# Kernel optimization log

Measured on AMD Instinct MI355X. Metric: run time of the kernel, lower is better.

## Reference

```python
import jax, jax.numpy as jnp
import numpy as np
import math

N = 50000      # nodes
E = 800000     # edges
IN = 64        # in_channels
HID = 128      # hidden_channels
OUT = 64       # out_channels
RATIO = 0.8
K = int(math.ceil(RATIO * N))  # 40000 nodes kept after TopKPooling


def setup_inputs() -> dict:
    key = jax.random.key(0)
    ks = jax.random.split(key, 12)
    x = jax.random.normal(ks[0], (N, IN), jnp.float32)
    edge_index = jax.random.randint(ks[1], (2, E), 0, N, dtype=jnp.int32)
    batch = jnp.zeros((N,), jnp.int32)  # single graph

    def glorot(k, fi, fo):
        return jax.random.normal(k, (fi, fo), jnp.float32) * (1.0 / np.sqrt(fi))

    W1 = glorot(ks[2], IN, HID);  b1 = jnp.zeros((HID,), jnp.float32)
    pool_w = jax.random.normal(ks[3], (HID,), jnp.float32) * (1.0 / np.sqrt(HID))
    W2 = glorot(ks[4], HID, OUT); b2 = jnp.zeros((OUT,), jnp.float32)
    W3 = glorot(ks[5], OUT, HID); b3 = jnp.zeros((HID,), jnp.float32)
    W4 = glorot(ks[6], HID, IN);  b4 = jnp.zeros((IN,), jnp.float32)
    return dict(x=x, edge_index=edge_index, batch=batch,
                W1=W1, b1=b1, pool_w=pool_w, W2=W2, b2=b2,
                W3=W3, b3=b3, W4=W4, b4=b4)


def gcn_conv(x, src, dst, ew, W, b, n):
    """PyG GCNConv: D^{-1/2}(A+I)D^{-1/2} X W + b; ew is a 0/1 edge mask."""
    h = x @ W                                             # [n, d_out]
    deg = 1.0 + jax.ops.segment_sum(ew, dst, num_segments=n)  # self-loop adds 1
    dis = jax.lax.rsqrt(deg)
    norm = dis[src] * dis[dst] * ew                       # [E]
    agg = jax.ops.segment_sum(norm[:, None] * h[src], dst, num_segments=n)
    agg = agg + h * (dis * dis)[:, None]                  # self-loop: norm = 1/deg
    return agg + b


def reference(x, edge_index, batch, W1, b1, pool_w, W2, b2, W3, b3, W4, b4):
    src, dst = edge_index[0], edge_index[1]
    ew = jnp.ones((E,), x.dtype)

    # conv1 + relu
    h = jax.nn.relu(gcn_conv(x, src, dst, ew, W1, b1, N))

    # TopKPooling(ratio=0.8): score = tanh(x.w/||w||), keep top-K, scale x by score
    score = jnp.tanh(h @ pool_w / jnp.linalg.norm(pool_w))  # [N]
    vals, perm = jax.lax.top_k(score, K)
    hp = h[perm] * vals[:, None]                            # [K, HID]
    # remap edges to pooled node ids; drop edges touching removed nodes via mask
    new_idx = jnp.full((N,), -1, jnp.int32).at[perm].set(jnp.arange(K, dtype=jnp.int32))
    ns, nd = new_idx[src], new_idx[dst]
    valid = ((ns >= 0) & (nd >= 0)).astype(x.dtype)
    ns = jnp.maximum(ns, 0)
    nd = jnp.maximum(nd, 0)

    h2 = jax.nn.relu(gcn_conv(hp, ns, nd, valid, W2, b2, K))
    h3 = jax.nn.relu(gcn_conv(h2, ns, nd, valid, W3, b3, K))
    h4 = gcn_conv(h3, ns, nd, valid, W4, b4, K)             # [K, IN]

    # global_mean_pool over the (single) graph -> [1, IN]
    return jnp.mean(h4, axis=0, keepdims=True)
```

## Files before the change

### kernel.cpp

```cpp
#include <hip/hip_runtime.h>
#include <hip/hip_bf16.h>
#include <stdint.h>

#define N_NODES 50000
#define N_EDGES 800000
#define K_KEEP  40000
#define BKT     196
#define BCAP    6144

typedef unsigned long long u64;
typedef unsigned int u32;
typedef unsigned short u16;
typedef __hip_bfloat16 bf16;
typedef __hip_bfloat162 bf16x2;
typedef __attribute__((ext_vector_type(8))) short short8;
typedef __attribute__((ext_vector_type(8))) unsigned short ushort8;
typedef __attribute__((ext_vector_type(4))) float f32x4;

struct Ctl {
  u64 prefix;
  u32 kremain;
  u32 cnt;
  float inv_norm;
  u32 isfp32;
  u32 done;
  u32 pad;
  u32 gen;
  u32 done2;
  u32 hist[256];
};

__device__ __forceinline__ float bf2f(bf16 v) { return __bfloat162float(v); }
__device__ __forceinline__ float bfbits2f(unsigned short u) {
  return __uint_as_float(((u32)u) << 16);
}
__device__ __forceinline__ float loadF(const void* p, size_t i, bool f32) {
  return f32 ? ((const float*)p)[i] : bf2f(((const bf16*)p)[i]);
}
__device__ __forceinline__ short f2bf_bits(float f) {
  bf16 t = __float2bfloat16(f);
  return *(const short*)&t;
}

__device__ __forceinline__ void gather_row8(const ushort8* __restrict__ H, int d, int lane,
                                            const int* __restrict__ rowstart,
                                            const int* __restrict__ len,
                                            const int* __restrict__ csr,
                                            const float* __restrict__ dis,
                                            int relusrc, float* acc)
{
  float dd = dis[d];
  float sw = dd * dd;
  ushort8 v = H[(size_t)d * 8 + lane];
  #pragma unroll
  for (int c = 0; c < 8; ++c) {
    float t = bfbits2f(v[c]);
    if (relusrc) t = fmaxf(t, 0.f);
    acc[c] = t * sw;
  }
  int i = rowstart[d];
  int i1 = len ? (i + len[d]) : rowstart[d + 1];
  for (; i + 4 <= i1; i += 4) {
    int s0 = csr[i], s1 = csr[i + 1], s2 = csr[i + 2], s3 = csr[i + 3];
    float w0 = dd * dis[s0], w1 = dd * dis[s1], w2 = dd * dis[s2], w3 = dd * dis[s3];
    ushort8 v0 = H[(size_t)s0 * 8 + lane];
    ushort8 v1 = H[(size_t)s1 * 8 + lane];
    ushort8 v2 = H[(size_t)s2 * 8 + lane];
    ushort8 v3 = H[(size_t)s3 * 8 + lane];
    #pragma unroll
    for (int c = 0; c < 8; ++c) {
      float x0 = bfbits2f(v0[c]), x1 = bfbits2f(v1[c]);
      float x2 = bfbits2f(v2[c]), x3 = bfbits2f(v3[c]);
      if (relusrc) {
        x0 = fmaxf(x0, 0.f); x1 = fmaxf(x1, 0.f);
        x2 = fmaxf(x2, 0.f); x3 = fmaxf(x3, 0.f);
      }
      acc[c] += w0 * x0 + w1 * x1 + w2 * x2 + w3 * x3;
    }
  }
  for (; i < i1; ++i) {
    int s = csr[i];
    float w = dd * dis[s];
    ushort8 vv = H[(size_t)s * 8 + lane];
    #pragma unroll
    for (int c = 0; c < 8; ++c) {
      float xx = bfbits2f(vv[c]);
      if (relusrc) xx = fmaxf(xx, 0.f);
      acc[c] += w * xx;
    }
  }
}


__global__ void init_kernel(const unsigned short* __restrict__ x16,
                            int* __restrict__ bucket_cur, int* __restrict__ detcnt, Ctl* ctl) {
  __shared__ u32 dsh[256];
  int i = blockIdx.x * 256 + threadIdx.x;
  if (i < BKT) bucket_cur[i] = i * BCAP;
  if (blockIdx.x == 0) {
    ctl->hist[threadIdx.x] = 0u;
    if (threadIdx.x == 0) {
      ctl->prefix = 0ull; ctl->kremain = K_KEEP; ctl->cnt = 0u;
      ctl->done = 0u; ctl->pad = 0u; ctl->gen = 0u; ctl->done2 = 0u;
    }
  }
  if (blockIdx.x < 64) {
    int base = blockIdx.x * 2048;
    u32 c = 0;
    for (int j = threadIdx.x; j < 2048; j += 256) {
      u32 h = x16[base + j];
      if ((h & 0x7F80u) == 0x7F80u) c++;
    }
    dsh[threadIdx.x] = c;
    __syncthreads();
    for (int s = 128; s > 0; s >>= 1) {
      if (threadIdx.x < s) dsh[threadIdx.x] += dsh[threadIdx.x + s];
      __syncthreads();
    }
    if (threadIdx.x == 0) detcnt[blockIdx.x] = (int)dsh[0];
  }
}


__global__ void bucket_scatter_kernel(const int* __restrict__ src, const int* __restrict__ dst,
                                      int* __restrict__ bucket_cur, u32* __restrict__ bucketbuf,
                                      const void* __restrict__ x, u32* __restrict__ xbf,
                                      const int* __restrict__ detcnt, const void* __restrict__ pw,
                                      Ctl* ctl)
{
  __shared__ u32 hist[BKT];
  __shared__ u32 base[BKT];
  __shared__ int f32sh;
  __shared__ float ns[128];
  const int tid = threadIdx.x;
  const int e0 = blockIdx.x * 2048;

  if (tid < 64) {
    int dc = detcnt[tid];
    for (int off = 32; off; off >>= 1) dc += __shfl_down(dc, off);
    if (tid == 0) f32sh = (dc >= 16) ? 1 : 0;
  }
  for (int t = tid; t < BKT; t += 256) hist[t] = 0;
  __syncthreads();
  const bool f32in = f32sh != 0;

  #pragma unroll
  for (int j = 0; j < 8; ++j) {
    int e = e0 + j * 256 + tid;
    if (e < N_EDGES) atomicAdd(&hist[dst[e] >> 8], 1u);
  }
  __syncthreads();
  for (int t = tid; t < BKT; t += 256) {
    u32 c = hist[t];
    base[t] = c ? (u32)atomicAdd(&bucket_cur[t], (int)c) : 0u;
    hist[t] = 0;
  }
  __syncthreads();
  #pragma unroll
  for (int j = 0; j < 8; ++j) {
    int e = e0 + j * 256 + tid;
    if (e < N_EDGES) {
      int d = dst[e];
      int b = d >> 8;
      u32 pos = base[b] + atomicAdd(&hist[b], 1u);
      bucketbuf[pos] = ((u32)src[e] << 8) | (u32)(d & 255);
    }
  }
  if (f32in) {
    const int p0 = blockIdx.x * 4096;
    const float2* xf = (const float2*)x;
    for (int j = tid; j < 4096; j += 256) {
      int p = p0 + j;
      if (p < N_NODES * 32) {
        float2 v = xf[p];
        u32 w = ((u32)(u16)f2bf_bits(v.y) << 16) | (u32)(u16)f2bf_bits(v.x);
        xbf[p] = w;
      }
    }
  }
  if (blockIdx.x == 0) {
    if (tid < 128) { float v = loadF(pw, tid, f32in); ns[tid] = v * v; }
    __syncthreads();
    for (int s = 64; s > 0; s >>= 1) {
      if (tid < s) ns[tid] += ns[tid + s];
      __syncthreads();
    }
    if (tid == 0) {
      ctl->inv_norm = 1.0f / sqrtf(ns[0]);
      ctl->isfp32 = f32in ? 1u : 0u;
    }
  }
}


__global__ void csr_from_buckets_kernel(const u32* __restrict__ bucketbuf, const int* __restrict__ bucket_cur,
                                        int* __restrict__ rowstart, float* __restrict__ dis,
                                        int* __restrict__ csr)
{
  __shared__ u32 cnt[256];
  __shared__ u32 loc[256];
  __shared__ u32 cur[256];
  const int b = blockIdx.x;
  const int tid = threadIdx.x;

  int v = (tid < BKT) ? (bucket_cur[tid] - tid * BCAP) : 0;
  loc[tid] = (u32)v;
  __syncthreads();
  for (int off = 1; off < 256; off <<= 1) {
    u32 t = (tid >= off) ? loc[tid - off] : 0;
    __syncthreads();
    loc[tid] += t;
    __syncthreads();
  }
  const int bc = bucket_cur[b] - b * BCAP;
  const int off0 = (int)loc[b] - bc;
  if (b == BKT - 1 && tid == 0) rowstart[N_NODES] = (int)loc[BKT - 1];
  __syncthreads();

  const u32* buf = bucketbuf + (size_t)b * BCAP;
  cnt[tid] = 0;
  __syncthreads();
  for (int i = tid; i < bc; i += 256) atomicAdd(&cnt[buf[i] & 255u], 1u);
  __syncthreads();
  u32 c = cnt[tid];
  loc[tid] = c;
  __syncthreads();
  for (int off = 1; off < 256; off <<= 1) {
    u32 t = (tid >= off) ? loc[tid - off] : 0;
    __syncthreads();
    loc[tid] += t;
    __syncthreads();
  }
  int node = b * 256 + tid;
  u32 excl = loc[tid] - c;
  if (node < N_NODES) {
    rowstart[node] = off0 + (int)excl;
    dis[node] = rsqrtf(1.0f + (float)c);
  }
  cur[tid] = off0 + excl;
  __syncthreads();
  for (int i = tid; i < bc; i += 256) {
    u32 p = buf[i];
    u32 pos = atomicAdd(&cur[p & 255u], 1u);
    csr[pos] = (int)(p >> 8);
  }
}


__global__ void agg_gather64_kernel(const bf16* __restrict__ hW, const bf16* __restrict__ hWalt,
                                    const int* __restrict__ rowstart,
                                    const int* __restrict__ len, const int* __restrict__ csr,
                                    const float* __restrict__ dis,
                                    const void* __restrict__ b, const Ctl* __restrict__ ctl,
                                    bf16* __restrict__ agg, int M, int relusrc, int addbias)
{
  const bool f32 = ctl->isfp32 != 0;
  int gid = blockIdx.x * 256 + threadIdx.x;
  int d = gid >> 3;
  int lane = gid & 7;
  if (d >= M) return;
  const ushort8* H = (const ushort8*)(f32 ? hWalt : hW);
  float acc[8];
  gather_row8(H, d, lane, rowstart, len, csr, dis, relusrc, acc);
  if (addbias) {
    #pragma unroll
    for (int c = 0; c < 8; ++c) acc[c] += loadF(b, 8 * lane + c, f32);
  }
  ushort8 outv;
  #pragma unroll
  for (int c = 0; c < 8; ++c) outv[c] = (unsigned short)f2bf_bits(acc[c]);
  ((ushort8*)agg)[(size_t)d * 8 + lane] = outv;
}


__global__ void gemm_in_kernel(const bf16* __restrict__ x, const bf16* __restrict__ xbf,
                               const int* __restrict__ rowstart, const int* __restrict__ csr,
                               const float* __restrict__ dis,
                               const void* __restrict__ W, const void* __restrict__ b,
                               const void* __restrict__ pw,
                               bf16* __restrict__ Y, const Ctl* __restrict__ ctl,
                               float* __restrict__ score, u64* __restrict__ keys)
{
  __shared__ short Xs[64 * 72];
  __shared__ short Wt[128 * 72];
  __shared__ float bs[128];
  __shared__ float ps[128];
  const bool f32 = ctl->isfp32 != 0;
  const int tid = threadIdx.x;
  const int row0 = blockIdx.x * 64;

  for (int i = tid; i < 64 * 128; i += 256) {
    int k = i >> 7, n = i & 127;
    Wt[n * 72 + k] = f32 ? f2bf_bits(((const float*)W)[i]) : ((const short*)W)[i];
  }
  {
    const ushort8* H = (const ushort8*)(f32 ? xbf : x);
    for (int u = tid; u < 512; u += 256) {
      int r = u >> 3, lane = u & 7;
      int d = row0 + r;
      float acc[8];
      if (d < N_NODES) {
        gather_row8(H, d, lane, rowstart, nullptr, csr, dis, 0, acc);
      } else {
        #pragma unroll
        for (int c = 0; c < 8; ++c) acc[c] = 0.f;
      }
      short8 outv;
      #pragma unroll
      for (int c = 0; c < 8; ++c) outv[c] = f2bf_bits(acc[c]);
      *(short8*)&Xs[r * 72 + lane * 8] = outv;
    }
  }
  for (int i = tid; i < 128; i += 256) { bs[i] = loadF(b, i, f32); ps[i] = loadF(pw, i, f32); }
  __syncthreads();

  const int lane = tid & 63;
  const int w = tid >> 6;
  const int l16 = lane & 15;
  const int quad = lane >> 4;
  f32x4 acc[8];
  #pragma unroll
  for (int ct = 0; ct < 8; ++ct) acc[ct] = (f32x4){0.f, 0.f, 0.f, 0.f};
  const int arow = w * 16 + l16;
  #pragma unroll
  for (int kc = 0; kc < 2; ++kc) {
    short8 a = *(short8*)&Xs[arow * 72 + kc * 32 + quad * 8];
    #pragma unroll
    for (int ct = 0; ct < 8; ++ct) {
      short8 bb = *(short8*)&Wt[(ct * 16 + l16) * 72 + kc * 32 + quad * 8];
      acc[ct] = __builtin_amdgcn_mfma_f32_16x16x32_bf16(a, bb, acc[ct], 0, 0, 0);
    }
  }
  float inv_norm = ctl->inv_norm;
  #pragma unroll
  for (int r = 0; r < 4; ++r) {
    int gr = row0 + w * 16 + quad * 4 + r;
    float p = 0.f;
    #pragma unroll
    for (int ct = 0; ct < 8; ++ct) {
      int col = ct * 16 + l16;
      float h = acc[ct][r] + bs[col];
      if (gr < N_NODES) Y[(size_t)gr * 128 + col] = __float2bfloat16(h);
      p += fmaxf(h, 0.f) * ps[col];
    }
    p += __shfl_down(p, 8, 16);
    p += __shfl_down(p, 4, 16);
    p += __shfl_down(p, 2, 16);
    p += __shfl_down(p, 1, 16);
    if (l16 == 0 && gr < N_NODES) {
      float sc = tanhf(p * inv_norm);
      score[gr] = sc;
      u32 u = __float_as_uint(sc);
      u = (u & 0x80000000u) ? ~u : (u | 0x80000000u);
      keys[gr] = (((u64)u) << 16) | (u64)(0xFFFFu - (u32)gr);
    }
  }
}

__global__ void gemm_128_64_kernel(const bf16* __restrict__ X, const void* __restrict__ W,
                                   bf16* __restrict__ Y, const Ctl* __restrict__ ctl,
                                   int M, int relu_x,
                                   const int* __restrict__ kept, const float* __restrict__ score)
{
  __shared__ short Xs[64 * 136];
  __shared__ short Wt[64 * 136];
  __shared__ int keptS[64];
  __shared__ float scS[64];
  const bool f32 = ctl->isfp32 != 0;
  const int tid = threadIdx.x;
  const int row0 = blockIdx.x * 64;

  if (kept) {
    for (int i = tid; i < 64; i += 256) {
      int o = kept[row0 + i];
      keptS[i] = o;
      scS[i] = score[o];
    }
  }
  __syncthreads();

  for (int i = tid; i < 128 * 64; i += 256) {
    int k = i >> 6, n = i & 63;
    Wt[n * 136 + k] = f32 ? f2bf_bits(((const float*)W)[i]) : ((const short*)W)[i];
  }
  const u32* X2 = (const u32*)X;
  for (int p = tid; p < 64 * 64; p += 256) {
    int r = p >> 6, kp = p & 63;
    int srow = kept ? keptS[r] : (row0 + r);
    u32 v = X2[(size_t)srow * 64 + kp];
    if (relu_x) {
      if (v & 0x8000u) v &= 0xFFFF0000u;
      if (v & 0x80000000u) v &= 0x0000FFFFu;
    }
    if (kept) {
      bf16x2 h = *(bf16x2*)&v;
      float s = scS[r];
      bf16x2 o;
      o.x = __float2bfloat16(fmaxf(bf2f(h.x), 0.f) * s);
      o.y = __float2bfloat16(fmaxf(bf2f(h.y), 0.f) * s);
      v = *(u32*)&o;
    }
    *(u32*)&Xs[r * 136 + 2 * kp] = v;
  }
  __syncthreads();

  const int lane = tid & 63;
  const int w = tid >> 6;
  const int l16 = lane & 15;
  const int quad = lane >> 4;
  f32x4 acc[4];
  #pragma unroll
  for (int ct = 0; ct < 4; ++ct) acc[ct] = (f32x4){0.f, 0.f, 0.f, 0.f};
  const int arow = w * 16 + l16;
  #pragma unroll
  for (int kc = 0; kc < 4; ++kc) {
    short8 a = *(short8*)&Xs[arow * 136 + kc * 32 + quad * 8];
    #pragma unroll
    for (int ct = 0; ct < 4; ++ct) {
      short8 bb = *(short8*)&Wt[(ct * 16 + l16) * 136 + kc * 32 + quad * 8];
      acc[ct] = __builtin_amdgcn_mfma_f32_16x16x32_bf16(a, bb, acc[ct], 0, 0, 0);
    }
  }
  #pragma unroll
  for (int ct = 0; ct < 4; ++ct)
    #pragma unroll
    for (int r = 0; r < 4; ++r) {
      int gr = row0 + w * 16 + quad * 4 + r;
      Y[(size_t)gr * 64 + ct * 16 + l16] = __float2bfloat16(acc[ct][r]);
    }
}

__global__ void gemm_64_128_kernel(const bf16* __restrict__ X,
                                   const int* __restrict__ rowstart, const int* __restrict__ len,
                                   const int* __restrict__ csr, const float* __restrict__ dis,
                                   const void* __restrict__ W, const void* __restrict__ b,
                                   bf16* __restrict__ Y, const Ctl* __restrict__ ctl, int M)
{
  __shared__ short Xs[64 * 72];
  __shared__ short Wt[128 * 72];
  __shared__ float bs[128];
  const bool f32 = ctl->isfp32 != 0;
  const int tid = threadIdx.x;
  const int row0 = blockIdx.x * 64;

  for (int i = tid; i < 64 * 128; i += 256) {
    int k = i >> 7, n = i & 127;
    Wt[n * 72 + k] = f32 ? f2bf_bits(((const float*)W)[i]) : ((const short*)W)[i];
  }
  {
    const ushort8* H = (const ushort8*)X;
    for (int u = tid; u < 512; u += 256) {
      int r = u >> 3, lane = u & 7;
      int d = row0 + r;
      float acc[8];
      gather_row8(H, d, lane, rowstart, len, csr, dis, 1, acc);
      short8 outv;
      #pragma unroll
      for (int c = 0; c < 8; ++c) outv[c] = f2bf_bits(acc[c]);
      *(short8*)&Xs[r * 72 + lane * 8] = outv;
    }
  }
  for (int i = tid; i < 128; i += 256) bs[i] = loadF(b, i, f32);
  __syncthreads();

  const int lane = tid & 63;
  const int w = tid >> 6;
  const int l16 = lane & 15;
  const int quad = lane >> 4;
  f32x4 acc[8];
  #pragma unroll
  for (int ct = 0; ct < 8; ++ct) acc[ct] = (f32x4){0.f, 0.f, 0.f, 0.f};
  const int arow = w * 16 + l16;
  #pragma unroll
  for (int kc = 0; kc < 2; ++kc) {
    short8 a = *(short8*)&Xs[arow * 72 + kc * 32 + quad * 8];
    #pragma unroll
    for (int ct = 0; ct < 8; ++ct) {
      short8 bb = *(short8*)&Wt[(ct * 16 + l16) * 72 + kc * 32 + quad * 8];
      acc[ct] = __builtin_amdgcn_mfma_f32_16x16x32_bf16(a, bb, acc[ct], 0, 0, 0);
    }
  }
  #pragma unroll
  for (int ct = 0; ct < 8; ++ct)
    #pragma unroll
    for (int r = 0; r < 4; ++r) {
      int gr = row0 + w * 16 + quad * 4 + r;
      int col = ct * 16 + l16;
      Y[(size_t)gr * 128 + col] = __float2bfloat16(acc[ct][r] + bs[col]);
    }
}

__global__ void agg_gather64_final_kernel(const bf16* __restrict__ hW, const int* __restrict__ rowstart,
                                          const int* __restrict__ len, const int* __restrict__ csr,
                                          const float* __restrict__ dis,
                                          float* __restrict__ partial, int M, int nblk)
{
  __shared__ float cs[64];
  const int tid = threadIdx.x;
  if (tid < 64) cs[tid] = 0.f;
  __syncthreads();
  const int lane = tid & 7;
  const ushort8* H = (const ushort8*)hW;
  float acc[8];
  #pragma unroll
  for (int c = 0; c < 8; ++c) acc[c] = 0.f;
  for (int d = (blockIdx.x * 256 + tid) >> 3; d < M; d += nblk * 32) {
    float dd = dis[d];
    float sw = dd * dd;
    ushort8 v = H[(size_t)d * 8 + lane];
    #pragma unroll
    for (int c = 0; c < 8; ++c) acc[c] += bfbits2f(v[c]) * sw;
    int i = rowstart[d];
    int i1 = i + len[d];
    for (; i + 4 <= i1; i += 4) {
      int s0 = csr[i], s1 = csr[i + 1], s2 = csr[i + 2], s3 = csr[i + 3];
      float w0 = dd * dis[s0], w1 = dd * dis[s1], w2 = dd * dis[s2], w3 = dd * dis[s3];
      ushort8 v0 = H[(size_t)s0 * 8 + lane];
      ushort8 v1 = H[(size_t)s1 * 8 + lane];
      ushort8 v2 = H[(size_t)s2 * 8 + lane];
      ushort8 v3 = H[(size_t)s3 * 8 + lane];
      #pragma unroll
      for (int c = 0; c < 8; ++c) {
        acc[c] += w0 * bfbits2f(v0[c]) + w1 * bfbits2f(v1[c])
                + w2 * bfbits2f(v2[c]) + w3 * bfbits2f(v3[c]);
      }
    }
    for (; i < i1; ++i) {
      int s = csr[i];
      float w = dd * dis[s];
      ushort8 vv = H[(size_t)s * 8 + lane];
      #pragma unroll
      for (int c = 0; c < 8; ++c) acc[c] += w * bfbits2f(vv[c]);
    }
  }
  #pragma unroll
  for (int c = 0; c < 8; ++c) atomicAdd(&cs[8 * lane + c], acc[c]);
  __syncthreads();
  if (tid < 64) partial[(size_t)tid * nblk + blockIdx.x] = cs[tid];
}

__global__ void reduce_out_kernel(const float* __restrict__ partial, const void* __restrict__ b,
                                  const Ctl* __restrict__ ctl, void* __restrict__ out, int nblk)
{
  __shared__ float sh[256];
  int c = blockIdx.x;
  float s = 0.f;
  for (int j = threadIdx.x; j < nblk; j += 256) s += partial[(size_t)c * nblk + j];
  sh[threadIdx.x] = s;
  __syncthreads();
  for (int st = 128; st > 0; st >>= 1) {
    if (threadIdx.x < st) sh[threadIdx.x] += sh[threadIdx.x + st];
    __syncthreads();
  }
  if (threadIdx.x == 0) {
    const bool f32 = ctl->isfp32 != 0;
    float val = sh[0] / (float)K_KEEP + loadF(b, c, f32);
    if (f32) ((float*)out)[c] = val;
    else     ((bf16*)out)[c] = __float2bfloat16(val);
  }
}


__global__ void histpick_kernel(const u64* __restrict__ keys, Ctl* ctl, int shift, int nblocks) {
  __shared__ u32 lh[256];
  __shared__ u32 sfx[256];
  __shared__ int lastflag;
  __shared__ int selsh;
  const int tid = threadIdx.x;
  if (ctl->gen != 0u) return;
  lh[tid] = 0;
  __syncthreads();
  u64 prefix = ctl->prefix;
  int i = blockIdx.x * 256 + tid;
  if (i < N_NODES) {
    u64 key = keys[i];
    if ((key >> (shift + 8)) == (prefix >> (shift + 8)))
      atomicAdd(&lh[(u32)((key >> shift) & 0xFF)], 1u);
  }
  __syncthreads();
  u32 c = lh[tid];
  if (c) atomicAdd(&ctl->hist[tid], c);
  __syncthreads();
  if (tid == 0) {
    __threadfence();
    u32 old = atomicAdd(&ctl->done, 1u);
    lastflag = (old == (u32)(nblocks - 1));
  }
  __syncthreads();
  if (!lastflag) return;
  u32 cc = atomicExch(&ctl->hist[tid], 0u);
  sfx[tid] = cc;
  __syncthreads();
  for (int off = 1; off < 256; off <<= 1) {
    u32 t = (tid + off < 256) ? sfx[tid + off] : 0u;
    __syncthreads();
    sfx[tid] += t;
    __syncthreads();
  }
  u32 kr = ctl->kremain;
  u32 above = (tid < 255) ? sfx[tid + 1] : 0u;
  if (sfx[tid] >= kr && above < kr) selsh = tid;
  __syncthreads();
  if (tid == 0) {
    int sel = selsh;
    u32 ab = (sel < 255) ? sfx[sel + 1] : 0u;
    u32 newkr = kr - ab;
    u32 bucketcnt = sfx[sel] - ab;
    ctl->kremain = newkr;
    ctl->prefix = prefix | (((u64)(u32)sel) << shift);
    if (newkr == bucketcnt) ctl->gen = 1u;
    ctl->done = 0u;
  }
}

__global__ void mark_kernel(const u64* __restrict__ keys, Ctl* ctl,
                            int* __restrict__ new_idx, int* __restrict__ kept)
{
  int i = blockIdx.x * 256 + threadIdx.x;
  if (i >= N_NODES) return;
  if (keys[i] >= ctl->prefix) {
    int pos = (int)atomicAdd(&ctl->cnt, 1u);
    new_idx[i] = pos;
    kept[pos] = i;
  } else {
    new_idx[i] = -1;
  }
}


__global__ void csr2_build_kernel(const int* __restrict__ kept, const int* __restrict__ rowstart1,
                                  const int* __restrict__ csr1, const int* __restrict__ new_idx,
                                  Ctl* ctl, int* __restrict__ rowstart2, int* __restrict__ len2,
                                  float* __restrict__ dis2, int* __restrict__ csr2)
{
  int kp = blockIdx.x * 256 + threadIdx.x;
  int lane = threadIdx.x & 63;
  int c = 0;
  int i0 = 0, i1 = 0;
  if (kp < K_KEEP) {
    int o = kept[kp];
    i0 = rowstart1[o]; i1 = rowstart1[o + 1];
    int i = i0;
    for (; i + 4 <= i1; i += 4) {
      int s0 = csr1[i], s1 = csr1[i + 1], s2 = csr1[i + 2], s3 = csr1[i + 3];
      c += (new_idx[s0] >= 0) + (new_idx[s1] >= 0) + (new_idx[s2] >= 0) + (new_idx[s3] >= 0);
    }
    for (; i < i1; ++i) c += (new_idx[csr1[i]] >= 0);
  }
  int pre = c;
  #pragma unroll
  for (int off = 1; off < 64; off <<= 1) {
    int t = __shfl_up(pre, off);
    if (lane >= off) pre += t;
  }
  int wtot = __shfl(pre, 63);
  int wbase = 0;
  if (lane == 0) wbase = (int)atomicAdd(&ctl->pad, (u32)wtot);
  wbase = __shfl(wbase, 0);
  int base = wbase + pre - c;
  if (kp < K_KEEP) {
    rowstart2[kp] = base;
    len2[kp] = c;
    dis2[kp] = rsqrtf(1.0f + (float)c);
    int w = base;
    for (int i = i0; i < i1; ++i) {
      int ns = new_idx[csr1[i]];
      if (ns >= 0) csr2[w++] = ns;
    }
  }
}


extern "C" void kernel_launch(void* const* d_in, const int* in_sizes, int n_in,
                              void* d_out, int out_size, void* d_ws, size_t ws_size,
                              hipStream_t stream)
{
  const void* x  = d_in[0];
  const int*  ei = (const int*)d_in[1];
  const void* W1 = d_in[3];
  const void* b1 = d_in[4];
  const void* pw = d_in[5];
  const void* W2 = d_in[6];
  const void* b2 = d_in[7];
  const void* W3 = d_in[8];
  const void* b3 = d_in[9];
  const void* W4 = d_in[10];
  const void* b4 = d_in[11];

  const int* src = ei;
  const int* dst = ei + N_EDGES;

  float* F = (float*)d_ws;
  bf16*  A16       = (bf16*)F;
  bf16*  B16       = (bf16*)(F + 3200000);
  bf16*  C16       = (bf16*)(F + 6400000);
  u32*   xbf       = (u32*)(F + 9000000);
  float* dis1      = F + 10600000;
  float* dis2      = F + 10650000;
  float* score     = F + 10690000;
  u64*   keys      = (u64*)(F + 10740000);
  int*   new_idx   = (int*)(F + 10840000);
  int*   kept      = (int*)(F + 10890000);
  int*   len2      = (int*)(F + 10930000);
  int*   rowstart1 = (int*)(F + 10970000);
  int*   rowstart2 = (int*)(F + 11020004);
  int*   csr1      = (int*)(F + 11060008);
  int*   csr2      = (int*)(F + 11860008);
  Ctl*   ctl       = (Ctl*)(F + 12660008);
  int*   detcnt    = (int*)(F + 12660856);
  int*   bucket_cur= (int*)(F + 12660920);
  u32*   bucketbuf = (u32*)(F + 12726908);
  float* partial   = F + 13931132;

  const int NB1 = (N_NODES + 255) / 256;
  const int EB2 = (N_EDGES + 2047) / 2048;
  const int GB1 = (N_NODES + 63) / 64;
  const int ABK = K_KEEP * 8 / 256;
  const int CB2 = (K_KEEP + 255) / 256;
  const int NBF = 1024;

  init_kernel<<<NB1, 256, 0, stream>>>((const unsigned short*)x, bucket_cur, detcnt, ctl);

  bucket_scatter_kernel<<<EB2, 256, 0, stream>>>(src, dst, bucket_cur, bucketbuf, x, xbf,
                                                 detcnt, pw, ctl);
  csr_from_buckets_kernel<<<BKT, 256, 0, stream>>>(bucketbuf, bucket_cur, rowstart1, dis1, csr1);

  gemm_in_kernel<<<GB1, 256, 0, stream>>>((const bf16*)x, (const bf16*)xbf, rowstart1, csr1, dis1,
                                          W1, b1, pw, B16, ctl, score, keys);

  for (int p = 0; p < 6; ++p)
    histpick_kernel<<<NB1, 256, 0, stream>>>(keys, ctl, 40 - 8 * p, NB1);
  mark_kernel<<<NB1, 256, 0, stream>>>(keys, ctl, new_idx, kept);

  csr2_build_kernel<<<CB2, 256, 0, stream>>>(kept, rowstart1, csr1, new_idx, ctl,
                                             rowstart2, len2, dis2, csr2);

  gemm_128_64_kernel<<<K_KEEP / 64, 256, 0, stream>>>(B16, W2, A16, ctl, K_KEEP, 0, kept, score);
  agg_gather64_kernel<<<ABK, 256, 0, stream>>>(A16, A16, rowstart2, len2, csr2, dis2, b2, ctl, C16, K_KEEP, 0, 1);

  gemm_64_128_kernel<<<K_KEEP / 64, 256, 0, stream>>>(C16, rowstart2, len2, csr2, dis2,
                                                      W3, b3, B16, ctl, K_KEEP);

  gemm_128_64_kernel<<<K_KEEP / 64, 256, 0, stream>>>(B16, W4, A16, ctl, K_KEEP, 1, nullptr, nullptr);
  agg_gather64_final_kernel<<<NBF, 256, 0, stream>>>(A16, rowstart2, len2, csr2, dis2,
                                                     partial, K_KEEP, NBF);
  reduce_out_kernel<<<64, 256, 0, stream>>>(partial, b4, ctl, d_out, NBF);
}
```

Baseline: 327.0 us.

## Prescale node features by deg^-1/2 to drop per-edge normalization gathers

Refactors GCN normalization so each source row is stored already multiplied by its dis value, and the destination scale is applied once per row. The gather loops then become plain sums, with no per-edge dis[src] loads or multiplies. The fp32-to-bf16 conversion of x moves from the bucket scatter kernel into the CSR build kernel, where it also applies the prescale. Rounding the prescaled values to bf16 shifts numerics slightly, and relu plus scaling are now folded into epilogues, so correctness depends on every producer applying the scale consistently.

```diff
diff --git a/kernel.cpp b/kernel.cpp
--- a/kernel.cpp
+++ b/kernel.cpp
@@ -42,52 +42,34 @@
   return *(const short*)&t;
 }
 
-__device__ __forceinline__ void gather_row8(const ushort8* __restrict__ H, int d, int lane,
-                                            const int* __restrict__ rowstart,
-                                            const int* __restrict__ len,
-                                            const int* __restrict__ csr,
-                                            const float* __restrict__ dis,
-                                            int relusrc, float* acc)
-{
-  float dd = dis[d];
-  float sw = dd * dd;
+__device__ __forceinline__ void gather_row8_pre(const ushort8* __restrict__ H, int d, int lane,
+                                                const int* __restrict__ rowstart,
+                                                const int* __restrict__ len,
+                                                const int* __restrict__ csr,
+                                                float* acc)
+{
   ushort8 v = H[(size_t)d * 8 + lane];
   #pragma unroll
-  for (int c = 0; c < 8; ++c) {
-    float t = bfbits2f(v[c]);
-    if (relusrc) t = fmaxf(t, 0.f);
-    acc[c] = t * sw;
-  }
+  for (int c = 0; c < 8; ++c) acc[c] = bfbits2f(v[c]);
   int i = rowstart[d];
   int i1 = len ? (i + len[d]) : rowstart[d + 1];
   for (; i + 4 <= i1; i += 4) {
     int s0 = csr[i], s1 = csr[i + 1], s2 = csr[i + 2], s3 = csr[i + 3];
-    float w0 = dd * dis[s0], w1 = dd * dis[s1], w2 = dd * dis[s2], w3 = dd * dis[s3];
     ushort8 v0 = H[(size_t)s0 * 8 + lane];
     ushort8 v1 = H[(size_t)s1 * 8 + lane];
     ushort8 v2 = H[(size_t)s2 * 8 + lane];
     ushort8 v3 = H[(size_t)s3 * 8 + lane];
     #pragma unroll
     for (int c = 0; c < 8; ++c) {
-      float x0 = bfbits2f(v0[c]), x1 = bfbits2f(v1[c]);
-      float x2 = bfbits2f(v2[c]), x3 = bfbits2f(v3[c]);
-      if (relusrc) {
-        x0 = fmaxf(x0, 0.f); x1 = fmaxf(x1, 0.f);
-        x2 = fmaxf(x2, 0.f); x3 = fmaxf(x3, 0.f);
-      }
-      acc[c] += w0 * x0 + w1 * x1 + w2 * x2 + w3 * x3;
+      acc[c] += (bfbits2f(v0[c]) + bfbits2f(v1[c]))
+              + (bfbits2f(v2[c]) + bfbits2f(v3[c]));
     }
   }
   for (; i < i1; ++i) {
     int s = csr[i];
-    float w = dd * dis[s];
     ushort8 vv = H[(size_t)s * 8 + lane];
     #pragma unroll
-    for (int c = 0; c < 8; ++c) {
-      float xx = bfbits2f(vv[c]);
-      if (relusrc) xx = fmaxf(xx, 0.f);
-      acc[c] += w * xx;
-    }
+    for (int c = 0; c < 8; ++c) acc[c] += bfbits2f(vv[c]);
   }
 }
 
@@ -124,7 +106,6 @@
 
 __global__ void bucket_scatter_kernel(const int* __restrict__ src, const int* __restrict__ dst,
                                       int* __restrict__ bucket_cur, u32* __restrict__ bucketbuf,
-                                      const void* __restrict__ x, u32* __restrict__ xbf,
                                       const int* __restrict__ detcnt, const void* __restrict__ pw,
                                       Ctl* ctl)
 {
@@ -166,18 +147,6 @@
       bucketbuf[pos] = ((u32)src[e] << 8) | (u32)(d & 255);
     }
   }
-  if (f32in) {
-    const int p0 = blockIdx.x * 4096;
-    const float2* xf = (const float2*)x;
-    for (int j = tid; j < 4096; j += 256) {
-      int p = p0 + j;
-      if (p < N_NODES * 32) {
-        float2 v = xf[p];
-        u32 w = ((u32)(u16)f2bf_bits(v.y) << 16) | (u32)(u16)f2bf_bits(v.x);
-        xbf[p] = w;
-      }
-    }
-  }
   if (blockIdx.x == 0) {
     if (tid < 128) { float v = loadF(pw, tid, f32in); ns[tid] = v * v; }
     __syncthreads();
@@ -195,11 +164,14 @@
 
 __global__ void csr_from_buckets_kernel(const u32* __restrict__ bucketbuf, const int* __restrict__ bucket_cur,
                                         int* __restrict__ rowstart, float* __restrict__ dis,
-                                        int* __restrict__ csr)
+                                        int* __restrict__ csr,
+                                        const void* __restrict__ x, ushort8* __restrict__ xbf,
+                                        const Ctl* __restrict__ ctl)
 {
   __shared__ u32 cnt[256];
   __shared__ u32 loc[256];
   __shared__ u32 cur[256];
+  __shared__ float disS[256];
   const int b = blockIdx.x;
   const int tid = threadIdx.x;
 
@@ -233,9 +205,11 @@
   }
   int node = b * 256 + tid;
   u32 excl = loc[tid] - c;
+  float ddv = rsqrtf(1.0f + (float)c);
+  disS[tid] = ddv;
   if (node < N_NODES) {
     rowstart[node] = off0 + (int)excl;
-    dis[node] = rsqrtf(1.0f + (float)c);
+    dis[node] = ddv;
   }
   cur[tid] = off0 + excl;
   __syncthreads();
@@ -244,36 +218,68 @@
     u32 pos = atomicAdd(&cur[p & 255u], 1u);
     csr[pos] = (int)(p >> 8);
   }
-}
-
-
-__global__ void agg_gather64_kernel(const bf16* __restrict__ hW, const bf16* __restrict__ hWalt,
-                                    const int* __restrict__ rowstart,
-                                    const int* __restrict__ len, const int* __restrict__ csr,
-                                    const float* __restrict__ dis,
-                                    const void* __restrict__ b, const Ctl* __restrict__ ctl,
-                                    bf16* __restrict__ agg, int M, int relusrc, int addbias)
+  {
+    const bool f32in = ctl->isfp32 != 0;
+    if (f32in) {
+      const float* xf = (const float*)x;
+      for (int u = tid; u < 2048; u += 256) {
+        int r = u >> 3, lane = u & 7;
+        int d = b * 256 + r;
+        if (d < N_NODES) {
+          float sc = disS[r];
+          ushort8 o;
+          #pragma unroll
+          for (int c2 = 0; c2 < 8; ++c2)
+            o[c2] = (u16)f2bf_bits(xf[(size_t)d * 64 + lane * 8 + c2] * sc);
+          xbf[(size_t)d * 8 + lane] = o;
+        }
+      }
+    } else {
+      const ushort8* xi = (const ushort8*)x;
+      for (int u = tid; u < 2048; u += 256) {
+        int r = u >> 3, lane = u & 7;
+        int d = b * 256 + r;
+        if (d < N_NODES) {
+          float sc = disS[r];
+          ushort8 vv = xi[(size_t)d * 8 + lane];
+          ushort8 o;
+          #pragma unroll
+          for (int c2 = 0; c2 < 8; ++c2)
+            o[c2] = (u16)f2bf_bits(bfbits2f(vv[c2]) * sc);
+          xbf[(size_t)d * 8 + lane] = o;
+        }
+      }
+    }
+  }
+}
+
+
+__global__ void gather_h2_kernel(const bf16* __restrict__ P, const int* __restrict__ rowstart,
+                                 const int* __restrict__ len, const int* __restrict__ csr,
+                                 const float* __restrict__ dis,
+                                 const void* __restrict__ b, const Ctl* __restrict__ ctl,
+                                 bf16* __restrict__ P2, int M)
 {
   const bool f32 = ctl->isfp32 != 0;
   int gid = blockIdx.x * 256 + threadIdx.x;
   int d = gid >> 3;
   int lane = gid & 7;
   if (d >= M) return;
-  const ushort8* H = (const ushort8*)(f32 ? hWalt : hW);
+  const ushort8* H = (const ushort8*)P;
   float acc[8];
-  gather_row8(H, d, lane, rowstart, len, csr, dis, relusrc, acc);
-  if (addbias) {
-    #pragma unroll
-    for (int c = 0; c < 8; ++c) acc[c] += loadF(b, 8 * lane + c, f32);
-  }
+  gather_row8_pre(H, d, lane, rowstart, len, csr, acc);
+  float dd = dis[d];
   ushort8 outv;
   #pragma unroll
-  for (int c = 0; c < 8; ++c) outv[c] = (unsigned short)f2bf_bits(acc[c]);
-  ((ushort8*)agg)[(size_t)d * 8 + lane] = outv;
-}
-
-
-__global__ void gemm_in_kernel(const bf16* __restrict__ x, const bf16* __restrict__ xbf,
+  for (int c = 0; c < 8; ++c) {
+    float h = acc[c] * dd + loadF(b, 8 * lane + c, f32);
+    outv[c] = (u16)f2bf_bits(fmaxf(h, 0.f) * dd);
+  }
+  ((ushort8*)P2)[(size_t)d * 8 + lane] = outv;
+}
+
+
+__global__ void gemm_in_kernel(const ushort8* __restrict__ xbf,
                                const int* __restrict__ rowstart, const int* __restrict__ csr,
                                const float* __restrict__ dis,
                                const void* __restrict__ W, const void* __restrict__ b,
@@ -293,23 +299,21 @@
     int k = i >> 7, n = i & 127;
     Wt[n * 72 + k] = f32 ? f2bf_bits(((const float*)W)[i]) : ((const short*)W)[i];
   }
-  {
-    const ushort8* H = (const ushort8*)(f32 ? xbf : x);
-    for (int u = tid; u < 512; u += 256) {
-      int r = u >> 3, lane = u & 7;
-      int d = row0 + r;
-      float acc[8];
-      if (d < N_NODES) {
-        gather_row8(H, d, lane, rowstart, nullptr, csr, dis, 0, acc);
-      } else {
-        #pragma unroll
-        for (int c = 0; c < 8; ++c) acc[c] = 0.f;
-      }
-      short8 outv;
+  for (int u = tid; u < 512; u += 256) {
+    int r = u >> 3, lane = u & 7;
+    int d = row0 + r;
+    float acc[8];
+    short8 outv;
+    if (d < N_NODES) {
+      gather_row8_pre(xbf, d, lane, rowstart, nullptr, csr, acc);
+      float dd = dis[d];
       #pragma unroll
-      for (int c = 0; c < 8; ++c) outv[c] = f2bf_bits(acc[c]);
-      *(short8*)&Xs[r * 72 + lane * 8] = outv;
-    }
+      for (int c = 0; c < 8; ++c) outv[c] = f2bf_bits(acc[c] * dd);
+    } else {
+      #pragma unroll
+      for (int c = 0; c < 8; ++c) outv[c] = 0;
+    }
+    *(short8*)&Xs[r * 72 + lane * 8] = outv;
   }
   for (int i = tid; i < 128; i += 256) { bs[i] = loadF(b, i, f32); ps[i] = loadF(pw, i, f32); }
   __syncthreads();
@@ -360,7 +364,8 @@
 __global__ void gemm_128_64_kernel(const bf16* __restrict__ X, const void* __restrict__ W,
                                    bf16* __restrict__ Y, const Ctl* __restrict__ ctl,
                                    int M, int relu_x,
-                                   const int* __restrict__ kept, const float* __restrict__ score)
+                                   const int* __restrict__ kept, const float* __restrict__ score,
+                                   const float* __restrict__ prescale)
 {
   __shared__ short Xs[64 * 136];
   __shared__ short Wt[64 * 136];
@@ -426,11 +431,13 @@
     #pragma unroll
     for (int r = 0; r < 4; ++r) {
       int gr = row0 + w * 16 + quad * 4 + r;
-      Y[(size_t)gr * 64 + ct * 16 + l16] = __float2bfloat16(acc[ct][r]);
-    }
-}
-
-__global__ void gemm_64_128_kernel(const bf16* __restrict__ X,
+      float val = acc[ct][r];
+      if (prescale) val *= prescale[gr];
+      Y[(size_t)gr * 64 + ct * 16 + l16] = __float2bfloat16(val);
+    }
+}
+
+__global__ void gemm_64_128_kernel(const bf16* __restrict__ P2,
                                    const int* __restrict__ rowstart, const int* __restrict__ len,
                                    const int* __restrict__ csr, const float* __restrict__ dis,
                                    const void* __restrict__ W, const void* __restrict__ b,
@@ -448,15 +455,16 @@
     Wt[n * 72 + k] = f32 ? f2bf_bits(((const float*)W)[i]) : ((const short*)W)[i];
   }
   {
-    const ushort8* H = (const ushort8*)X;
+    const ushort8* H = (const ushort8*)P2;
     for (int u = tid; u < 512; u += 256) {
       int r = u >> 3, lane = u & 7;
       int d = row0 + r;
       float acc[8];
-      gather_row8(H, d, lane, rowstart, len, csr, dis, 1, acc);
+      gather_row8_pre(H, d, lane, rowstart, len, csr, acc);
+      float dd = dis[d];
       short8 outv;
       #pragma unroll
-      for (int c = 0; c < 8; ++c) outv[c] = f2bf_bits(acc[c]);
+      for (int c = 0; c < 8; ++c) outv[c] = f2bf_bits(acc[c] * dd);
       *(short8*)&Xs[r * 72 + lane * 8] = outv;
     }
   }
@@ -490,7 +498,7 @@
     }
 }
 
-__global__ void agg_gather64_final_kernel(const bf16* __restrict__ hW, const int* __restrict__ rowstart,
+__global__ void agg_gather64_final_kernel(const bf16* __restrict__ P, const int* __restrict__ rowstart,
                                           const int* __restrict__ len, const int* __restrict__ csr,
                                           const float* __restrict__ dis,
                                           float* __restrict__ partial, int M, int nblk)
@@ -500,38 +508,16 @@
   if (tid < 64) cs[tid] = 0.f;
   __syncthreads();
   const int lane = tid & 7;
-  const ushort8* H = (const ushort8*)hW;
+  const ushort8* H = (const ushort8*)P;
   float acc[8];
   #pragma unroll
   for (int c = 0; c < 8; ++c) acc[c] = 0.f;
   for (int d = (blockIdx.x * 256 + tid) >> 3; d < M; d += nblk * 32) {
+    float rsum[8];
+    gather_row8_pre(H, d, lane, rowstart, len, csr, rsum);
     float dd = dis[d];
-    float sw = dd * dd;
-    ushort8 v = H[(size_t)d * 8 + lane];
-    #pragma unroll
-    for (int c = 0; c < 8; ++c) acc[c] += bfbits2f(v[c]) * sw;
-    int i = rowstart[d];
-    int i1 = i + len[d];
-    for (; i + 4 <= i1; i += 4) {
-      int s0 = csr[i], s1 = csr[i + 1], s2 = csr[i + 2], s3 = csr[i + 3];
-      float w0 = dd * dis[s0], w1 = dd * dis[s1], w2 = dd * dis[s2], w3 = dd * dis[s3];
-      ushort8 v0 = H[(size_t)s0 * 8 + lane];
-      ushort8 v1 = H[(size_t)s1 * 8 + lane];
-      ushort8 v2 = H[(size_t)s2 * 8 + lane];
-      ushort8 v3 = H[(size_t)s3 * 8 + lane];
-      #pragma unroll
-      for (int c = 0; c < 8; ++c) {
-        acc[c] += w0 * bfbits2f(v0[c]) + w1 * bfbits2f(v1[c])
-                + w2 * bfbits2f(v2[c]) + w3 * bfbits2f(v3[c]);
-      }
-    }
-    for (; i < i1; ++i) {
-      int s = csr[i];
-      float w = dd * dis[s];
-      ushort8 vv = H[(size_t)s * 8 + lane];
-      #pragma unroll
-      for (int c = 0; c < 8; ++c) acc[c] += w * bfbits2f(vv[c]);
-    }
+    #pragma unroll
+    for (int c = 0; c < 8; ++c) acc[c] += rsum[c] * dd;
   }
   #pragma unroll
   for (int c = 0; c < 8; ++c) atomicAdd(&cs[8 * lane + c], acc[c]);
@@ -721,11 +707,12 @@
 
   init_kernel<<<NB1, 256, 0, stream>>>((const unsigned short*)x, bucket_cur, detcnt, ctl);
 
-  bucket_scatter_kernel<<<EB2, 256, 0, stream>>>(src, dst, bucket_cur, bucketbuf, x, xbf,
+  bucket_scatter_kernel<<<EB2, 256, 0, stream>>>(src, dst, bucket_cur, bucketbuf,
                                                  detcnt, pw, ctl);
-  csr_from_buckets_kernel<<<BKT, 256, 0, stream>>>(bucketbuf, bucket_cur, rowstart1, dis1, csr1);
-
-  gemm_in_kernel<<<GB1, 256, 0, stream>>>((const bf16*)x, (const bf16*)xbf, rowstart1, csr1, dis1,
+  csr_from_buckets_kernel<<<BKT, 256, 0, stream>>>(bucketbuf, bucket_cur, rowstart1, dis1, csr1,
+                                                   x, (ushort8*)xbf, ctl);
+
+  gemm_in_kernel<<<GB1, 256, 0, stream>>>((const ushort8*)xbf, rowstart1, csr1, dis1,
                                           W1, b1, pw, B16, ctl, score, keys);
 
   for (int p = 0; p < 6; ++p)
@@ -735,13 +722,13 @@
   csr2_build_kernel<<<CB2, 256, 0, stream>>>(kept, rowstart1, csr1, new_idx, ctl,
                                              rowstart2, len2, dis2, csr2);
 
-  gemm_128_64_kernel<<<K_KEEP / 64, 256, 0, stream>>>(B16, W2, A16, ctl, K_KEEP, 0, kept, score);
-  agg_gather64_kernel<<<ABK, 256, 0, stream>>>(A16, A16, rowstart2, len2, csr2, dis2, b2, ctl, C16, K_KEEP, 0, 1);
+  gemm_128_64_kernel<<<K_KEEP / 64, 256, 0, stream>>>(B16, W2, A16, ctl, K_KEEP, 0, kept, score, dis2);
+  gather_h2_kernel<<<ABK, 256, 0, stream>>>(A16, rowstart2, len2, csr2, dis2, b2, ctl, C16, K_KEEP);
 
   gemm_64_128_kernel<<<K_KEEP / 64, 256, 0, stream>>>(C16, rowstart2, len2, csr2, dis2,
                                                       W3, b3, B16, ctl, K_KEEP);
 
-  gemm_128_64_kernel<<<K_KEEP / 64, 256, 0, stream>>>(B16, W4, A16, ctl, K_KEEP, 1, nullptr, nullptr);
+  gemm_128_64_kernel<<<K_KEEP / 64, 256, 0, stream>>>(B16, W4, A16, ctl, K_KEEP, 1, nullptr, nullptr, dis2);
   agg_gather64_final_kernel<<<NBF, 256, 0, stream>>>(A16, rowstart2, len2, csr2, dis2,
                                                      partial, K_KEEP, NBF);
   reduce_out_kernel<<<64, 256, 0, stream>>>(partial, b4, ctl, d_out, NBF);
```

Result: faster. 319.4 us (-2.3%).
